# Optimization experiments

Hardware: AMD Instinct MI355X
Metric: run time of the kernel (lower is better)

Reference implementation:

```python
import jax, jax.numpy as jnp
import numpy as np

N = 100000   # nodes
E = 1600000  # edges
IN = 128     # input feature dim
HID = 64     # hidden = IN // 2
OUT = 8      # output_size
B = 16384    # lookup batch


def sage_conv(x, src, dst, W_l, W_r, b, n):
    # PyG SAGEConv (aggr='mean', root_weight=True):
    # out = lin_l(mean_{j in N(i)} x_j) + lin_r(x_i)
    msgs = x[src]                                              # [E, F] gather
    agg = jax.ops.segment_sum(msgs, dst, num_segments=n)       # [N, F] scatter-add
    deg = jax.ops.segment_sum(jnp.ones((src.shape[0],), x.dtype), dst, num_segments=n)
    mean = agg / jnp.maximum(deg, 1.0)[:, None]                # zero-degree -> 0
    return mean @ W_l + x @ W_r + b


def setup_inputs() -> dict:
    key = jax.random.key(0)
    ks = jax.random.split(key, 10)
    node_feats = jax.random.normal(ks[0], (N, IN), dtype=jnp.float32)
    edge_index = jax.random.randint(ks[1], (2, E), 0, N, dtype=jnp.int64)
    idx = jax.random.randint(ks[2], (B,), 0, N, dtype=jnp.int64)
    dropout_mask = jax.random.uniform(ks[3], (N, HID), dtype=jnp.float32)
    s1 = 1.0 / np.sqrt(IN)
    s2 = 1.0 / np.sqrt(HID)
    W1_l = jax.random.normal(ks[4], (IN, HID), dtype=jnp.float32) * s1
    W1_r = jax.random.normal(ks[5], (IN, HID), dtype=jnp.float32) * s1
    b1 = jnp.zeros((HID,), dtype=jnp.float32)
    W2_l = jax.random.normal(ks[6], (HID, OUT), dtype=jnp.float32) * s2
    W2_r = jax.random.normal(ks[7], (HID, OUT), dtype=jnp.float32) * s2
    b2 = jnp.zeros((OUT,), dtype=jnp.float32)
    return {"node_feats": node_feats, "edge_index": edge_index, "idx": idx,
            "dropout_mask": dropout_mask, "W1_l": W1_l, "W1_r": W1_r, "b1": b1,
            "W2_l": W2_l, "W2_r": W2_r, "b2": b2}


def reference(node_feats, edge_index, idx, dropout_mask, W1_l, W1_r, b1, W2_l, W2_r, b2):
    n = node_feats.shape[0]
    src, dst = edge_index[0], edge_index[1]
    h = sage_conv(node_feats, src, dst, W1_l, W1_r, b1, n)     # [N, HID]
    h = jax.nn.relu(h)
    keep = (dropout_mask > 0.5).astype(h.dtype)                # F.dropout p=0.5
    h = h * keep * 2.0                                         # inverted dropout scale 1/(1-p)
    emb = sage_conv(h, src, dst, W2_l, W2_r, b2, n)            # [N, OUT]
    return emb[idx]                                            # [B, OUT]
```

## Files before the change

kernel.cpp:

```cpp
#include <hip/hip_runtime.h>
#include <hip/hip_fp16.h>

#define IN_F 128
#define HID_F 64
#define OUT_F 8

#define BSHIFT 7
#define BGRAN 128
#define BCAP 2688
#define NBUK_MAX 784
#define CHUNK 4096
#define EPT (CHUNK / 256)
#define CEPT ((BCAP + 255) / 256)

typedef _Float16 f16x8 __attribute__((ext_vector_type(8)));
typedef float f32x4 __attribute__((ext_vector_type(4)));

__global__ __launch_bounds__(1024) void init_bcur(int* __restrict__ bcur, int nbuk) {
  int t = threadIdx.x;
  if (t < nbuk) bcur[t] = t * BCAP;
}

__global__ __launch_bounds__(256) void bucket_scatter(
    const int* __restrict__ src, const int* __restrict__ dst,
    int* __restrict__ bcur, int* __restrict__ ebuf, int n_edges) {
  __shared__ int hist[NBUK_MAX];
  __shared__ int base[NBUK_MAX];
  int t = threadIdx.x;
  for (int i = t; i < NBUK_MAX; i += 256) hist[i] = 0;
  __syncthreads();
  int e0 = blockIdx.x * CHUNK;
  int pk[EPT];
  int bk[EPT];
#pragma unroll
  for (int k = 0; k < EPT; ++k) {
    int e = e0 + k * 256 + t;
    if (e < n_edges) {
      int s = src[e];
      int d = dst[e];
      bk[k] = d >> BSHIFT;
      pk[k] = ((d & (BGRAN - 1)) << 24) | s;
      atomicAdd(&hist[bk[k]], 1);
    } else {
      bk[k] = -1;
    }
  }
  __syncthreads();
  for (int i = t; i < NBUK_MAX; i += 256) {
    int c = hist[i];
    base[i] = c ? atomicAdd(&bcur[i], c) : 0;
  }
  __syncthreads();
  for (int i = t; i < NBUK_MAX; i += 256) hist[i] = 0;
  __syncthreads();
#pragma unroll
  for (int k = 0; k < EPT; ++k) {
    if (bk[k] >= 0) {
      int r = atomicAdd(&hist[bk[k]], 1);
      ebuf[base[bk[k]] + r] = pk[k];
    }
  }
}

__global__ __launch_bounds__(256) void bucket_csr(
    const int* __restrict__ ebuf, const int* __restrict__ bcur,
    uint2* __restrict__ nd, int* __restrict__ csr_src, int n_nodes) {
  __shared__ int hist[BGRAN];
  __shared__ int cur[BGRAN];
  __shared__ int excl_s[BGRAN];
  __shared__ int lds_src[BCAP];
  int b = blockIdx.x;
  int t = threadIdx.x;
  if (t < BGRAN) hist[t] = 0;
  __syncthreads();
  int beg = b * BCAP;
  int cnt = bcur[b] - beg;
  int pk[CEPT];
  int np = 0;
  for (int j = t; j < cnt; j += 256) {
    pk[np] = ebuf[beg + j];
    atomicAdd(&hist[(unsigned)pk[np] >> 24], 1);
    ++np;
  }
  __syncthreads();
  if (t < 64) {
    int h0 = hist[2 * t];
    int h1 = hist[2 * t + 1];
    int ps = h0 + h1;
#pragma unroll
    for (int dd = 1; dd < 64; dd <<= 1) {
      int u = __shfl_up(ps, dd);
      if (t >= dd) ps += u;
    }
    excl_s[2 * t] = ps - h1 - h0;
    excl_s[2 * t + 1] = ps - h1;
  }
  __syncthreads();
  if (t < BGRAN) {
    int excl = excl_s[t];
    cur[t] = excl;
    int node = b * BGRAN + t;
    if (node < n_nodes) nd[node] = make_uint2((unsigned)(beg + excl), (unsigned)hist[t]);
  }
  __syncthreads();
  for (int i = 0; i < np; ++i) {
    int dl = (unsigned)pk[i] >> 24;
    int p = atomicAdd(&cur[dl], 1);
    lds_src[p] = pk[i] & 0xFFFFFF;
  }
  __syncthreads();
  for (int j = t; j < cnt; j += 256) csr_src[beg + j] = lds_src[j];
}

__global__ __launch_bounds__(128) void w_prep(
    const float* __restrict__ Wl, const float* __restrict__ Wr,
    _Float16* __restrict__ Wt) {
  int n = threadIdx.x;
  for (int k = 0; k < IN_F; ++k) {
    float v = (n < HID_F) ? Wl[k * HID_F + n] : Wr[k * HID_F + (n - HID_F)];
    Wt[n * IN_F + k] = (_Float16)v;
  }
}

#define K1_ROWS 128
#define XSH 136
__global__ __launch_bounds__(256) void k1_proj(
    const float* __restrict__ x,
    const _Float16* __restrict__ Wt,
    const float* __restrict__ b1,
    const float* __restrict__ mask,
    __half* __restrict__ y1h,
    __half* __restrict__ r1h,
    unsigned long long* __restrict__ mbits,
    int n_nodes) {
  __shared__ _Float16 XS[K1_ROWS * XSH];
  int tid = threadIdx.x;
  int w = tid >> 6;
  int lane = tid & 63;
  int n0 = blockIdx.x * K1_ROWS;
  int m = lane & 15;
  int quad = lane >> 4;

#pragma unroll
  for (int i0 = 0; i0 < 32; i0 += 8) {
    float mv[8];
#pragma unroll
    for (int u = 0; u < 8; ++u) {
      int node = n0 + w * 32 + i0 + u;
      mv[u] = (node < n_nodes) ? mask[(size_t)node * HID_F + lane] : 0.f;
    }
#pragma unroll
    for (int u = 0; u < 8; ++u) {
      int node = n0 + w * 32 + i0 + u;
      unsigned long long bits = __ballot(mv[u] > 0.5f);
      if (lane == 0 && node < n_nodes) mbits[node] = bits;
    }
  }

  f16x8 af[2][4];
#pragma unroll
  for (int ti = 0; ti < 2; ++ti) {
    int t = w + ti * 4;
#pragma unroll
    for (int kk = 0; kk < 4; ++kk)
      af[ti][kk] = *(const f16x8*)(Wt + (size_t)(t * 16 + m) * IN_F + kk * 32 + quad * 8);
  }
  float4 b1v = *(const float4*)(b1 + w * 16 + quad * 4);

#pragma unroll
  for (int p = 0; p < 16; ++p) {
    int i = tid + p * 256;
    int row = i >> 5;
    int k4 = (i & 31) * 4;
    int gs = min(n0 + row, n_nodes - 1);
    float4 v = *(const float4*)(x + (size_t)gs * IN_F + k4);
    _Float16 hv[4] = {(_Float16)v.x, (_Float16)v.y, (_Float16)v.z, (_Float16)v.w};
    *(uint2*)&XS[row * XSH + k4] = *(uint2*)hv;
  }
  __syncthreads();

#pragma unroll
  for (int rt = 0; rt < 8; ++rt) {
    f32x4 acc0 = f32x4{0.f, 0.f, 0.f, 0.f};
    f32x4 acc1 = f32x4{0.f, 0.f, 0.f, 0.f};
#pragma unroll
    for (int kk = 0; kk < 4; ++kk) {
      f16x8 bx = *(const f16x8*)&XS[(rt * 16 + m) * XSH + kk * 32 + quad * 8];
      acc0 = __builtin_amdgcn_mfma_f32_16x16x32_f16(af[0][kk], bx, acc0, 0, 0, 0);
      acc1 = __builtin_amdgcn_mfma_f32_16x16x32_f16(af[1][kk], bx, acc1, 0, 0, 0);
    }
    int node = n0 + rt * 16 + m;
    if (node < n_nodes) {
      __half hy[4], hr[4];
#pragma unroll
      for (int r = 0; r < 4; ++r) {
        hy[r] = __float2half(acc0[r]);
        hr[r] = __float2half(acc1[r] + ((const float*)&b1v)[r]);
      }
      *(uint2*)(y1h + (size_t)node * HID_F + w * 16 + quad * 4) = *(uint2*)hy;
      *(uint2*)(r1h + (size_t)node * HID_F + w * 16 + quad * 4) = *(uint2*)hr;
    }
  }
}

__global__ __launch_bounds__(256) void agg1_fused(
    const __half* __restrict__ y1h,
    const __half* __restrict__ r1h,
    const uint2* __restrict__ nd,
    const int* __restrict__ csr_src,
    const unsigned long long* __restrict__ mbits,
    __half* __restrict__ h_h,
    int n_nodes) {
  int node = (blockIdx.x * blockDim.x + threadIdx.x) >> 6;
  int lane = threadIdx.x & 63;
  if (node >= n_nodes) return;
  int nu = __builtin_amdgcn_readfirstlane(node);
  int q = lane >> 4;
  int f4 = lane & 15;

  uint2 be = nd[nu];
  unsigned long long mb = mbits[nu];
  size_t o = (size_t)nu * HID_F + f4 * 4;
  uint2 rg = *(const uint2*)(r1h + o);

  int beg = (int)be.x;
  int d = (int)be.y;
  const int* cp = csr_src + beg;
  float a0 = 0.f, a1 = 0.f, a2 = 0.f, a3 = 0.f;

#define ACC4(g)                                              \
  {                                                          \
    float2 p0 = __half22float2(*(const __half2*)&(g).x);     \
    float2 p1 = __half22float2(*(const __half2*)&(g).y);     \
    a0 += p0.x; a1 += p0.y; a2 += p1.x; a3 += p1.y;          \
  }

  int j = 0;
  for (; j + 32 <= d; j += 32) {
    int s0 = cp[j + q];
    int s1 = cp[j + 4 + q];
    int s2 = cp[j + 8 + q];
    int s3 = cp[j + 12 + q];
    int s4 = cp[j + 16 + q];
    int s5 = cp[j + 20 + q];
    int s6 = cp[j + 24 + q];
    int s7 = cp[j + 28 + q];
    uint2 g0 = *(const uint2*)(y1h + (size_t)s0 * HID_F + f4 * 4);
    uint2 g1 = *(const uint2*)(y1h + (size_t)s1 * HID_F + f4 * 4);
    uint2 g2 = *(const uint2*)(y1h + (size_t)s2 * HID_F + f4 * 4);
    uint2 g3 = *(const uint2*)(y1h + (size_t)s3 * HID_F + f4 * 4);
    uint2 g4 = *(const uint2*)(y1h + (size_t)s4 * HID_F + f4 * 4);
    uint2 g5 = *(const uint2*)(y1h + (size_t)s5 * HID_F + f4 * 4);
    uint2 g6 = *(const uint2*)(y1h + (size_t)s6 * HID_F + f4 * 4);
    uint2 g7 = *(const uint2*)(y1h + (size_t)s7 * HID_F + f4 * 4);
    ACC4(g0) ACC4(g1) ACC4(g2) ACC4(g3)
    ACC4(g4) ACC4(g5) ACC4(g6) ACC4(g7)
  }
  if (j + 16 <= d) {
    int s0 = cp[j + q];
    int s1 = cp[j + 4 + q];
    int s2 = cp[j + 8 + q];
    int s3 = cp[j + 12 + q];
    uint2 g0 = *(const uint2*)(y1h + (size_t)s0 * HID_F + f4 * 4);
    uint2 g1 = *(const uint2*)(y1h + (size_t)s1 * HID_F + f4 * 4);
    uint2 g2 = *(const uint2*)(y1h + (size_t)s2 * HID_F + f4 * 4);
    uint2 g3 = *(const uint2*)(y1h + (size_t)s3 * HID_F + f4 * 4);
    ACC4(g0) ACC4(g1) ACC4(g2) ACC4(g3)
    j += 16;
  }
  if (j < d) {
    int dm = d - 1;
    int e0 = j + q, e1 = j + 4 + q, e2 = j + 8 + q, e3 = j + 12 + q;
    int s0 = cp[min(e0, dm)];
    int s1 = cp[min(e1, dm)];
    int s2 = cp[min(e2, dm)];
    int s3 = cp[min(e3, dm)];
    uint2 g0 = *(const uint2*)(y1h + (size_t)s0 * HID_F + f4 * 4);
    uint2 g1 = *(const uint2*)(y1h + (size_t)s1 * HID_F + f4 * 4);
    uint2 g2 = *(const uint2*)(y1h + (size_t)s2 * HID_F + f4 * 4);
    uint2 g3 = *(const uint2*)(y1h + (size_t)s3 * HID_F + f4 * 4);
    if (e0 < d) ACC4(g0)
    if (e1 < d) ACC4(g1)
    if (e2 < d) ACC4(g2)
    if (e3 < d) ACC4(g3)
  }
#undef ACC4

  a0 += __shfl_xor(a0, 16); a0 += __shfl_xor(a0, 32);
  a1 += __shfl_xor(a1, 16); a1 += __shfl_xor(a1, 32);
  a2 += __shfl_xor(a2, 16); a2 += __shfl_xor(a2, 32);
  a3 += __shfl_xor(a3, 16); a3 += __shfl_xor(a3, 32);
  if (q == 0) {
    float inv = 1.0f / fmaxf((float)d, 1.0f);
    float2 r01 = __half22float2(*(const __half2*)&rg.x);
    float2 r23 = __half22float2(*(const __half2*)&rg.y);
    float vx = fmaxf(a0 * inv + r01.x, 0.f);
    float vy = fmaxf(a1 * inv + r01.y, 0.f);
    float vz = fmaxf(a2 * inv + r23.x, 0.f);
    float vw = fmaxf(a3 * inv + r23.y, 0.f);
    int fb = f4 * 4;
    vx = ((mb >> (fb + 0)) & 1ull) ? vx * 2.f : 0.f;
    vy = ((mb >> (fb + 1)) & 1ull) ? vy * 2.f : 0.f;
    vz = ((mb >> (fb + 2)) & 1ull) ? vz * 2.f : 0.f;
    vw = ((mb >> (fb + 3)) & 1ull) ? vw * 2.f : 0.f;
    __half hh[4] = {__float2half(vx), __float2half(vy),
                    __float2half(vz), __float2half(vw)};
    *(uint2*)(h_h + o) = *(uint2*)hh;
  }
}

__global__ __launch_bounds__(256) void k3b_z(
    const __half* __restrict__ h_h,
    const float* __restrict__ W2l,
    __half* __restrict__ z,
    int n_nodes) {
  __shared__ float WS[HID_F][OUT_F];
  int tid = threadIdx.x;
  if (tid < 128) {
    float4 w = *(const float4*)(W2l + tid * 4);
    *(float4*)&WS[tid >> 1][(tid & 1) * 4] = w;
  }
  __syncthreads();
  int node = blockIdx.x * blockDim.x + tid;
  if (node >= n_nodes) return;
  const __half* hr = h_h + (size_t)node * HID_F;
  float acc[8] = {0, 0, 0, 0, 0, 0, 0, 0};
  for (int k = 0; k < HID_F; k += 8) {
    uint4 hv = *(const uint4*)(hr + k);
    float2 f0 = __half22float2(*(const __half2*)&hv.x);
    float2 f1 = __half22float2(*(const __half2*)&hv.y);
    float2 f2 = __half22float2(*(const __half2*)&hv.z);
    float2 f3 = __half22float2(*(const __half2*)&hv.w);
    float hh[8] = {f0.x, f0.y, f1.x, f1.y, f2.x, f2.y, f3.x, f3.y};
#pragma unroll
    for (int j = 0; j < 8; ++j) {
      float4 w0 = *(const float4*)&WS[k + j][0];
      float4 w1 = *(const float4*)&WS[k + j][4];
      acc[0] += hh[j] * w0.x; acc[1] += hh[j] * w0.y;
      acc[2] += hh[j] * w0.z; acc[3] += hh[j] * w0.w;
      acc[4] += hh[j] * w1.x; acc[5] += hh[j] * w1.y;
      acc[6] += hh[j] * w1.z; acc[7] += hh[j] * w1.w;
    }
  }
  __half hz[8];
#pragma unroll
  for (int j = 0; j < 8; ++j) hz[j] = __float2half(acc[j]);
  *(uint4*)(z + (size_t)node * OUT_F) = *(uint4*)hz;
}

__global__ __launch_bounds__(256) void out_fused(
    const int* __restrict__ idx,
    const __half* __restrict__ z,
    const uint2* __restrict__ nd,
    const int* __restrict__ csr_src,
    const __half* __restrict__ h_h,
    const float* __restrict__ W2r,
    const float* __restrict__ b2,
    float* __restrict__ out,
    int n_batch) {
  int b = (blockIdx.x * blockDim.x + threadIdx.x) >> 6;
  int lane = threadIdx.x & 63;
  if (b >= n_batch) return;
  int bu = __builtin_amdgcn_readfirstlane(b);
  int i = idx[bu];
  int iu = __builtin_amdgcn_readfirstlane(i);
  int e8 = lane >> 3;
  int o = lane & 7;
  uint2 be = nd[iu];
  uint4 hv = *(const uint4*)(h_h + (size_t)iu * HID_F + e8 * 8);
  int beg = (int)be.x;
  int d = (int)be.y;
  const int* cp = csr_src + beg;
  float acc = 0.f;
  int j = e8;
  for (; j + 8 < d; j += 16) {
    int s0 = cp[j];
    int s1 = cp[j + 8];
    float z0 = __half2float(z[(size_t)s0 * OUT_F + o]);
    float z1 = __half2float(z[(size_t)s1 * OUT_F + o]);
    acc += z0 + z1;
  }
  if (j < d) acc += __half2float(z[(size_t)cp[j] * OUT_F + o]);
  float dv = fmaxf((float)d, 1.0f);
  float v = acc / dv;
  float2 f0 = __half22float2(*(const __half2*)&hv.x);
  float2 f1 = __half22float2(*(const __half2*)&hv.y);
  float2 f2 = __half22float2(*(const __half2*)&hv.z);
  float2 f3 = __half22float2(*(const __half2*)&hv.w);
  float hh[8] = {f0.x, f0.y, f1.x, f1.y, f2.x, f2.y, f3.x, f3.y};
#pragma unroll
  for (int jj = 0; jj < 8; ++jj) {
    int k = e8 * 8 + jj;
    v += hh[jj] * W2r[k * OUT_F + o];
  }
  v += __shfl_xor(v, 8);
  v += __shfl_xor(v, 16);
  v += __shfl_xor(v, 32);
  if (e8 == 0) out[(size_t)b * OUT_F + o] = v + b2[o];
}

extern "C" void kernel_launch(void* const* d_in, const int* in_sizes, int n_in,
                              void* d_out, int out_size, void* d_ws, size_t ws_size,
                              hipStream_t stream) {
  const float* x    = (const float*)d_in[0];
  const int*   ei   = (const int*)d_in[1];
  const int*   idx  = (const int*)d_in[2];
  const float* mask = (const float*)d_in[3];
  const float* W1l  = (const float*)d_in[4];
  const float* W1r  = (const float*)d_in[5];
  const float* b1   = (const float*)d_in[6];
  const float* W2l  = (const float*)d_in[7];
  const float* W2r  = (const float*)d_in[8];
  const float* b2   = (const float*)d_in[9];
  float* out = (float*)d_out;

  int n_nodes = in_sizes[0] / IN_F;
  int n_edges = in_sizes[1] / 2;
  int n_batch = in_sizes[2];
  const int* src = ei;
  const int* dst = ei + n_edges;

  int nbuk = (n_nodes + BGRAN - 1) / BGRAN;
  int nchunk = (n_edges + CHUNK - 1) / CHUNK;

  char* ws = (char*)d_ws;
  size_t off = 0;
  __half* y1h = (__half*)(ws + off); off += (size_t)n_nodes * HID_F * 2;
  __half* r1h = (__half*)(ws + off); off += (size_t)n_nodes * HID_F * 2;
  __half* h_h = (__half*)(ws + off); off += (size_t)n_nodes * HID_F * 2;
  __half* z   = (__half*)(ws + off); off += (size_t)n_nodes * OUT_F * 2;
  unsigned long long* mbits = (unsigned long long*)(ws + off); off += (size_t)n_nodes * 8;
  _Float16* Wt = (_Float16*)(ws + off); off += (size_t)IN_F * IN_F * 2;
  int* ebuf    = (int*)(ws + off); off += (size_t)nbuk * BCAP * 4;
  int* csr_src = (int*)(ws + off); off += (size_t)nbuk * BCAP * 4;
  uint2* nd    = (uint2*)(ws + off); off += (size_t)n_nodes * 8;
  int* bcur    = (int*)(ws + off); off += NBUK_MAX * 4;

  init_bcur<<<1, 1024, 0, stream>>>(bcur, nbuk);
  w_prep<<<1, 128, 0, stream>>>(W1l, W1r, Wt);
  bucket_scatter<<<nchunk, 256, 0, stream>>>(src, dst, bcur, ebuf, n_edges);
  k1_proj<<<(n_nodes + K1_ROWS - 1) / K1_ROWS, 256, 0, stream>>>(
      x, Wt, b1, mask, y1h, r1h, mbits, n_nodes);
  bucket_csr<<<nbuk, 256, 0, stream>>>(ebuf, bcur, nd, csr_src, n_nodes);

  {
    long long th = (long long)n_nodes * HID_F;
    agg1_fused<<<(int)((th + 255) / 256), 256, 0, stream>>>(
        y1h, r1h, nd, csr_src, mbits, h_h, n_nodes);
  }

  k3b_z<<<(n_nodes + 255) / 256, 256, 0, stream>>>(h_h, W2l, z, n_nodes);
  {
    long long th = (long long)n_batch * 64;
    out_fused<<<(int)((th + 255) / 256), 256, 0, stream>>>(
        idx, z, nd, csr_src, h_h, W2r, b2, out, n_batch);
  }
}
```

Baseline: 246.0 us.

## Split mask packing into own kernel, parallelize weight prep, halve k1 tile rows

Moves dropout-mask bit packing out of the projection kernel into a separate grid-stride kernel. The weight transpose/convert now runs across 16 blocks with vectorized stores instead of one block looping serially. The projection kernel now handles 64 rows per block instead of 128, which doubles its grid size and halves its shared-memory use. The aim is to remove a serial bottleneck and the mask-read latency from the MFMA kernel, at the cost of one extra kernel launch.

```diff
diff --git a/kernel.cpp b/kernel.cpp
--- a/kernel.cpp
+++ b/kernel.cpp
@@ -19,6 +19,40 @@
 __global__ __launch_bounds__(1024) void init_bcur(int* __restrict__ bcur, int nbuk) {
   int t = threadIdx.x;
   if (t < nbuk) bcur[t] = t * BCAP;
+}
+
+__global__ __launch_bounds__(256) void mask_pack(
+    const float* __restrict__ mask,
+    unsigned long long* __restrict__ mbits, int n_nodes) {
+  int wid = (blockIdx.x * 256 + threadIdx.x) >> 6;
+  int lane = threadIdx.x & 63;
+  int nw = (gridDim.x * 256) >> 6;
+  int step = nw * 4;
+  int node = wid * 4;
+  for (; node + 4 <= n_nodes; node += step) {
+    float m0 = mask[(size_t)(node + 0) * HID_F + lane];
+    float m1 = mask[(size_t)(node + 1) * HID_F + lane];
+    float m2 = mask[(size_t)(node + 2) * HID_F + lane];
+    float m3 = mask[(size_t)(node + 3) * HID_F + lane];
+    unsigned long long b0 = __ballot(m0 > 0.5f);
+    unsigned long long b1 = __ballot(m1 > 0.5f);
+    unsigned long long b2 = __ballot(m2 > 0.5f);
+    unsigned long long b3 = __ballot(m3 > 0.5f);
+    if (lane == 0) {
+      mbits[node + 0] = b0;
+      mbits[node + 1] = b1;
+      mbits[node + 2] = b2;
+      mbits[node + 3] = b3;
+    }
+  }
+  if (node < n_nodes) {
+    int rem = n_nodes - node;
+    for (int u = 0; u < rem; ++u) {
+      float mv = mask[(size_t)(node + u) * HID_F + lane];
+      unsigned long long bb = __ballot(mv > 0.5f);
+      if (lane == 0) mbits[node + u] = bb;
+    }
+  }
 }
 
 __global__ __launch_bounds__(256) void bucket_scatter(
@@ -112,26 +146,30 @@
   for (int j = t; j < cnt; j += 256) csr_src[beg + j] = lds_src[j];
 }
 
-__global__ __launch_bounds__(128) void w_prep(
+__global__ __launch_bounds__(256) void w_prep(
     const float* __restrict__ Wl, const float* __restrict__ Wr,
     _Float16* __restrict__ Wt) {
-  int n = threadIdx.x;
-  for (int k = 0; k < IN_F; ++k) {
-    float v = (n < HID_F) ? Wl[k * HID_F + n] : Wr[k * HID_F + (n - HID_F)];
-    Wt[n * IN_F + k] = (_Float16)v;
-  }
-}
-
-#define K1_ROWS 128
+  int i = blockIdx.x * 256 + threadIdx.x;
+  int n = i & 127;
+  int k4 = (i >> 7) * 4;
+  _Float16 hv[4];
+#pragma unroll
+  for (int j = 0; j < 4; ++j) {
+    float v = (n < HID_F) ? Wl[(k4 + j) * HID_F + n]
+                          : Wr[(k4 + j) * HID_F + (n - HID_F)];
+    hv[j] = (_Float16)v;
+  }
+  *(uint2*)(Wt + (size_t)n * IN_F + k4) = *(uint2*)hv;
+}
+
+#define K1_ROWS 64
 #define XSH 136
 __global__ __launch_bounds__(256) void k1_proj(
     const float* __restrict__ x,
     const _Float16* __restrict__ Wt,
     const float* __restrict__ b1,
-    const float* __restrict__ mask,
     __half* __restrict__ y1h,
     __half* __restrict__ r1h,
-    unsigned long long* __restrict__ mbits,
     int n_nodes) {
   __shared__ _Float16 XS[K1_ROWS * XSH];
   int tid = threadIdx.x;
@@ -141,22 +179,6 @@
   int m = lane & 15;
   int quad = lane >> 4;
 
-#pragma unroll
-  for (int i0 = 0; i0 < 32; i0 += 8) {
-    float mv[8];
-#pragma unroll
-    for (int u = 0; u < 8; ++u) {
-      int node = n0 + w * 32 + i0 + u;
-      mv[u] = (node < n_nodes) ? mask[(size_t)node * HID_F + lane] : 0.f;
-    }
-#pragma unroll
-    for (int u = 0; u < 8; ++u) {
-      int node = n0 + w * 32 + i0 + u;
-      unsigned long long bits = __ballot(mv[u] > 0.5f);
-      if (lane == 0 && node < n_nodes) mbits[node] = bits;
-    }
-  }
-
   f16x8 af[2][4];
 #pragma unroll
   for (int ti = 0; ti < 2; ++ti) {
@@ -168,7 +190,7 @@
   float4 b1v = *(const float4*)(b1 + w * 16 + quad * 4);
 
 #pragma unroll
-  for (int p = 0; p < 16; ++p) {
+  for (int p = 0; p < 8; ++p) {
     int i = tid + p * 256;
     int row = i >> 5;
     int k4 = (i & 31) * 4;
@@ -180,7 +202,7 @@
   __syncthreads();
 
 #pragma unroll
-  for (int rt = 0; rt < 8; ++rt) {
+  for (int rt = 0; rt < 4; ++rt) {
     f32x4 acc0 = f32x4{0.f, 0.f, 0.f, 0.f};
     f32x4 acc1 = f32x4{0.f, 0.f, 0.f, 0.f};
 #pragma unroll
@@ -437,10 +459,11 @@
   int* bcur    = (int*)(ws + off); off += NBUK_MAX * 4;
 
   init_bcur<<<1, 1024, 0, stream>>>(bcur, nbuk);
-  w_prep<<<1, 128, 0, stream>>>(W1l, W1r, Wt);
+  w_prep<<<16, 256, 0, stream>>>(W1l, W1r, Wt);
+  mask_pack<<<1024, 256, 0, stream>>>(mask, mbits, n_nodes);
   bucket_scatter<<<nchunk, 256, 0, stream>>>(src, dst, bcur, ebuf, n_edges);
   k1_proj<<<(n_nodes + K1_ROWS - 1) / K1_ROWS, 256, 0, stream>>>(
-      x, Wt, b1, mask, y1h, r1h, mbits, n_nodes);
+      x, Wt, b1, y1h, r1h, n_nodes);
   bucket_csr<<<nbuk, 256, 0, stream>>>(ebuf, bcur, nd, csr_src, n_nodes);
 
   {
```

Result: faster. 225.8 us (-8.2%).
